# Kernel tuning notes

Hardware: AMD Instinct MI355X
Metric: run time of the kernel (lower is better)

## Reference

```python
import jax, jax.numpy as jnp
import numpy as np

N, T, D = 32, 64, 16
F = 512  # object_classes == feature dim after object_fc


def _gcn(x, adj, W, b):
    # Kipf GraphConvolution: adj @ (x @ W) + b
    return adj @ (x @ W) + b


def _norm_adj(a):
    d = jnp.sum(a, axis=1) ** -0.5
    return a * d[:, None] * d[None, :]


def _per_graph(x, gc1_W, gc1_b, gc2_W, gc2_b, gc3_W, gc3_b, gc4_W, gc4_b):
    # x: [D, F]
    # graph_generator / adj2: softmax-style similarity adjacency with D^{-1/2} norm
    s = x @ x.T                                   # [D, D]
    a = jnp.exp(s - jnp.max(s, axis=1, keepdims=True))
    adj = _norm_adj(a)
    # branch 1
    x1 = jax.nn.relu(_gcn(x, adj, gc1_W, gc1_b))
    x1 = _gcn(x1, adj, gc2_W, gc2_b)
    # branch 2 (adj_hat2 identical construction from x)
    y2 = jax.nn.relu(_gcn(x, adj, gc3_W, gc3_b))  # [D, 32]
    y22 = y2 @ y2.T
    nrm = jnp.sqrt(jnp.sum(y22 * y22, axis=1, keepdims=True))  # torch.norm(y22, 2, dim=1)
    adj3 = 1.0 + y22 / (nrm @ nrm.T)
    adj_hat3 = _norm_adj(adj3)
    y2 = _gcn(y2, adj_hat3, gc4_W, gc4_b)
    return (x1 + y2) * 0.5


def setup_inputs() -> dict:
    key = jax.random.key(0)
    ks = jax.random.split(key, 12)
    s = 0.02
    return {
        "object_raw": jax.random.normal(ks[0], (N * T * D, F), jnp.float32),
        "action_raw": jax.random.normal(ks[1], (N * T, F), jnp.float32),
        "W_obj": jax.random.normal(ks[2], (F, 512), jnp.float32) * s,
        "b_obj": jnp.zeros((512,), jnp.float32),
        "W_act": jax.random.normal(ks[3], (F, 512), jnp.float32) * s,
        "b_act": jnp.zeros((512,), jnp.float32),
        "gc1_W": jax.random.normal(ks[4], (512, 32), jnp.float32) * s,
        "gc1_b": jnp.zeros((32,), jnp.float32),
        "gc2_W": jax.random.normal(ks[5], (32, 512), jnp.float32) * s,
        "gc2_b": jnp.zeros((512,), jnp.float32),
        "gc3_W": jax.random.normal(ks[6], (512, 32), jnp.float32) * s,
        "gc3_b": jnp.zeros((32,), jnp.float32),
        "gc4_W": jax.random.normal(ks[7], (32, 512), jnp.float32) * s,
        "gc4_b": jnp.zeros((512,), jnp.float32),
        "fc1_W": jax.random.normal(ks[8], (512, 1024), jnp.float32) * s,
        "fc1_b": jnp.zeros((1024,), jnp.float32),
        "clf_W": jax.random.normal(ks[9], (1024, 500), jnp.float32) * s,
        "clf_b": jnp.zeros((500,), jnp.float32),
    }


def reference(object_raw, action_raw, W_obj, b_obj, W_act, b_act,
              gc1_W, gc1_b, gc2_W, gc2_b, gc3_W, gc3_b, gc4_W, gc4_b,
              fc1_W, fc1_b, clf_W, clf_b):
    obj = jax.nn.relu(object_raw @ W_obj + b_obj).reshape(N * T, D, 512)
    act = jax.nn.relu(action_raw @ W_act + b_act)           # [N*T, 512]
    obj = obj.at[:, D // 2].set(act)                         # overwrite middle frame
    graph = jax.vmap(lambda x: _per_graph(x, gc1_W, gc1_b, gc2_W, gc2_b,
                                          gc3_W, gc3_b, gc4_W, gc4_b))(obj)
    g = graph.reshape(N, T, D, 512).mean(axis=2)
    o = obj.reshape(N, T, D, 512).mean(axis=2)
    feat = (o + g) * 0.5                                     # graph_fusion == 'mean'
    c = jax.nn.relu(feat)                                    # dropout = identity (eval)
    c = jax.nn.relu(c @ fc1_W + fc1_b)
    out = (c @ clf_W + clf_b).mean(axis=1)                   # mean over T -> [N, 500]
    return out
```

## Files before the change

### kernel.cpp

```cpp
#include <hip/hip_runtime.h>
#include <hip/hip_bf16.h>

using ushort_t = unsigned short;
using f32x4  = __attribute__((ext_vector_type(4))) float;
using short8 = __attribute__((ext_vector_type(8))) short;

__device__ __forceinline__ float bflo(unsigned p) {
    union { unsigned u; float f; } x; x.u = p << 16; return x.f;
}
__device__ __forceinline__ float bfhi(unsigned p) {
    union { unsigned u; float f; } x; x.u = p & 0xffff0000u; return x.f;
}
__device__ __forceinline__ ushort_t f2bf(float f) {
    __hip_bfloat16 h = __float2bfloat16(f);
    return *(ushort_t*)&h;
}
__device__ __forceinline__ unsigned pk2bf(float lo, float hi) {
    __hip_bfloat162 h = __float22bfloat162_rn({lo, hi});
    return *(unsigned*)&h;
}

__device__ __forceinline__ void tr_tile(const float* __restrict__ S, ushort_t* __restrict__ D,
                                        int K, int N, int Npad, int bx, int by,
                                        int tx, int ty, float* tile )
{
    const int k0 = by * 32, n0 = bx * 32;
#pragma unroll
    for (int r = 0; r < 4; r++) {
        const int k = k0 + ty + r * 8, n = n0 + tx;
        tile[(ty + r * 8) * 33 + tx] = (k < K && n < N) ? S[(size_t)k * N + n] : 0.f;
    }
    __syncthreads();
#pragma unroll
    for (int r = 0; r < 4; r++) {
        const int n = n0 + ty + r * 8, k = k0 + tx;
        if (n < Npad && k < K) D[(size_t)n * K + k] = f2bf(tile[tx * 33 + ty + r * 8]);
    }
}

__device__ __forceinline__ void trf_tile(const float* __restrict__ S, float* __restrict__ D,
                                         int K, int N, int bx, int by,
                                         int tx, int ty, float* tile )
{
    const int k0 = by * 32, n0 = bx * 32;
#pragma unroll
    for (int r = 0; r < 4; r++) {
        const int k = k0 + ty + r * 8, n = n0 + tx;
        tile[(ty + r * 8) * 33 + tx] = (k < K && n < N) ? S[(size_t)k * N + n] : 0.f;
    }
    __syncthreads();
#pragma unroll
    for (int r = 0; r < 4; r++) {
        const int n = n0 + ty + r * 8, k = k0 + tx;
        if (n < N && k < K) D[(size_t)n * K + k] = tile[tx * 33 + ty + r * 8];
    }
}

__global__ __launch_bounds__(256)
void prep_weights(const float* __restrict__ Wobj, ushort_t* __restrict__ WobjT,
                  const float* __restrict__ Wact, ushort_t* __restrict__ WactT,
                  const float* __restrict__ fc1W, ushort_t* __restrict__ fc1T,
                  const float* __restrict__ gc1W, ushort_t* __restrict__ W1t,
                  const float* __restrict__ gc3W, ushort_t* __restrict__ W3t,
                  const float* __restrict__ gc2W, ushort_t* __restrict__ W2bf,
                  const float* __restrict__ gc4W, ushort_t* __restrict__ W4bf,
                  const float* __restrict__ clfW, float* __restrict__ WclfT)
{
    __shared__ float tile[32 * 33];
    const int b = blockIdx.x;
    const int t = threadIdx.x;
    const int tx = t & 31, ty = t >> 5;

    if (b < 1056) {
        const float* S; ushort_t* D; int K, N, Npad, nt, l;
        if      (b < 256)  { S = Wobj; D = WobjT; K = 512; N = 512;  Npad = 512;  nt = 16; l = b; }
        else if (b < 512)  { S = Wact; D = WactT; K = 512; N = 512;  Npad = 512;  nt = 16; l = b - 256; }
        else if (b < 1024) { S = fc1W; D = fc1T;  K = 512; N = 1024; Npad = 1024; nt = 32; l = b - 512; }
        else if (b < 1040) { S = gc1W; D = W1t;   K = 512; N = 32;   Npad = 32;   nt = 1;  l = b - 1024; }
        else               { S = gc3W; D = W3t;   K = 512; N = 32;   Npad = 32;   nt = 1;  l = b - 1040; }
        tr_tile(S, D, K, N, Npad, l % nt, l / nt, tx, ty, tile);
    } else if (b < 1072) {
        const float* S = (b < 1064) ? gc2W : gc4W;
        ushort_t* D    = (b < 1064) ? W2bf : W4bf;
        const int i = (b < 1064 ? b - 1056 : b - 1064) * 256 + t;
        const float4 x = ((const float4*)S)[2 * i];
        const float4 y = ((const float4*)S)[2 * i + 1];
        unsigned r[4] = { pk2bf(x.x, x.y), pk2bf(x.z, x.w), pk2bf(y.x, y.y), pk2bf(y.z, y.w) };
        ((uint4*)D)[i] = *(uint4*)r;
    } else {
        const int l = b - 1072;
        trf_tile(clfW, WclfT, 1024, 500, l & 15, l >> 4, tx, ty, tile);
    }
}

typedef __attribute__((address_space(1))) void glb_void;
typedef __attribute__((address_space(3))) void lds_void;
__device__ __forceinline__ void dma16(const void* g, void* l) {
    __builtin_amdgcn_global_load_lds((glb_void*)(unsigned long long)(uintptr_t)g,
                                     (lds_void*)(unsigned)(uintptr_t)l, 16, 0, 0);
}

template<int RELU, typename AT>
__global__ __launch_bounds__(256)
void gemm_dma(const AT* __restrict__ A, const ushort_t* __restrict__ Bt,
              const float* __restrict__ bias, ushort_t* __restrict__ C,
              int N, int K, int Nb, int row_mul, int row_add)
{
    __shared__ __align__(16) char     AsRaw[128 * 32 * sizeof(AT)];
    __shared__ __align__(16) ushort_t Bs[128 * 32];
    const int t = threadIdx.x;
    const int lane = t & 63, w = t >> 6;
    const int bm = blockIdx.y * 128, bn = blockIdx.x * 128;
    const int mb = (w & 1) * 64, nb = (w >> 1) * 64;
    const int fr = lane & 15, fq = lane >> 4;

    f32x4 acc[16];
#pragma unroll
    for (int i = 0; i < 16; i++) acc[i] = (f32x4){0.f, 0.f, 0.f, 0.f};

    const int brow = lane >> 2, bk = lane & 3;
    const int klog = bk ^ ((brow >> 1) & 3);
    const int arow = lane >> 3, ag = lane & 7;

    for (int k0 = 0; k0 < K; k0 += 32) {
        __syncthreads();
        if constexpr (sizeof(AT) == 4) {
#pragma unroll
            for (int i = 0; i < 4; i++) {
                const int grp = w * 4 + i;
                const int row = grp * 8 + arow;
                const int gl = ag ^ (row & 7);
                dma16((const float*)A + (size_t)(bm + row) * K + k0 + gl * 4,
                      AsRaw + grp * 1024);
            }
        } else {
#pragma unroll
            for (int i = 0; i < 2; i++) {
                const int grp = w * 2 + i;
                const int row = grp * 16 + brow;
                dma16((const ushort_t*)A + (size_t)(bm + row) * K + k0 + klog * 8,
                      (ushort_t*)AsRaw + grp * 512);
            }
        }
#pragma unroll
        for (int i = 0; i < 2; i++) {
            const int grp = w * 2 + i;
            const int row = grp * 16 + brow;
            dma16(Bt + (size_t)(bn + row) * K + k0 + klog * 8, Bs + grp * 512);
        }
        __syncthreads();

        short8 af[4], bf[4];
        if constexpr (sizeof(AT) == 4) {
#pragma unroll
            for (int i = 0; i < 4; i++) {
                const int row = mb + i * 16 + fr;
                const float* base = (const float*)AsRaw + row * 32;
                const f32x4 p0 = *(const f32x4*)(base + (((2 * fq)     ^ (fr & 7)) * 4));
                const f32x4 p1 = *(const f32x4*)(base + (((2 * fq + 1) ^ (fr & 7)) * 4));
                unsigned rr[4] = { pk2bf(p0.x, p0.y), pk2bf(p0.z, p0.w),
                                   pk2bf(p1.x, p1.y), pk2bf(p1.z, p1.w) };
                af[i] = *(short8*)rr;
            }
        } else {
#pragma unroll
            for (int i = 0; i < 4; i++) {
                const int row = mb + i * 16 + fr;
                af[i] = *(const short8*)((const ushort_t*)AsRaw + row * 32 + (fq ^ ((fr >> 1) & 3)) * 8);
            }
        }
#pragma unroll
        for (int j = 0; j < 4; j++) {
            const int row = nb + j * 16 + fr;
            bf[j] = *(const short8*)(Bs + row * 32 + (fq ^ ((fr >> 1) & 3)) * 8);
        }
#pragma unroll
        for (int i = 0; i < 4; i++)
#pragma unroll
            for (int j = 0; j < 4; j++)
                acc[i * 4 + j] = __builtin_amdgcn_mfma_f32_16x16x32_bf16(
                    af[i], bf[j], acc[i * 4 + j], 0, 0, 0);
    }

#pragma unroll
    for (int j = 0; j < 4; j++) {
        const int n = bn + nb + j * 16 + fr;
        const float bv = (n < Nb) ? bias[n] : 0.f;
#pragma unroll
        for (int i = 0; i < 4; i++) {
            const f32x4 a = acc[i * 4 + j];
#pragma unroll
            for (int r = 0; r < 4; r++) {
                const int m = bm + mb + i * 16 + fq * 4 + r;
                float v = a[r] + bv;
                if (RELU) v = fmaxf(v, 0.f);
                C[((size_t)m * row_mul + row_add) * (size_t)N + n] = f2bf(v);
            }
        }
    }
}

__global__ __launch_bounds__(256)
void gemm_fc1_mean(const ushort_t* __restrict__ A, const ushort_t* __restrict__ Bt,
                   const float* __restrict__ bias, float* __restrict__ cmean)
{
    __shared__ __align__(16) ushort_t AsS[128 * 32];
    __shared__ __align__(16) ushort_t Bs[128 * 32];
    const int t = threadIdx.x;
    const int lane = t & 63, w = t >> 6;
    const int bm = blockIdx.y * 128, bn = blockIdx.x * 128;
    const int mb = (w & 1) * 64, nb = (w >> 1) * 64;
    const int fr = lane & 15, fq = lane >> 4;
    const int K = 512;

    f32x4 acc[16];
#pragma unroll
    for (int i = 0; i < 16; i++) acc[i] = (f32x4){0.f, 0.f, 0.f, 0.f};

    const int brow = lane >> 2, bk = lane & 3;
    const int klog = bk ^ ((brow >> 1) & 3);

    for (int k0 = 0; k0 < K; k0 += 32) {
        __syncthreads();
#pragma unroll
        for (int i = 0; i < 2; i++) {
            const int grp = w * 2 + i;
            const int row = grp * 16 + brow;
            dma16(A + (size_t)(bm + row) * K + k0 + klog * 8, AsS + grp * 512);
        }
#pragma unroll
        for (int i = 0; i < 2; i++) {
            const int grp = w * 2 + i;
            const int row = grp * 16 + brow;
            dma16(Bt + (size_t)(bn + row) * K + k0 + klog * 8, Bs + grp * 512);
        }
        __syncthreads();

        short8 af[4], bf[4];
#pragma unroll
        for (int i = 0; i < 4; i++) {
            const int row = mb + i * 16 + fr;
            af[i] = *(const short8*)(AsS + row * 32 + (fq ^ ((fr >> 1) & 3)) * 8);
        }
#pragma unroll
        for (int j = 0; j < 4; j++) {
            const int row = nb + j * 16 + fr;
            bf[j] = *(const short8*)(Bs + row * 32 + (fq ^ ((fr >> 1) & 3)) * 8);
        }
#pragma unroll
        for (int i = 0; i < 4; i++)
#pragma unroll
            for (int j = 0; j < 4; j++)
                acc[i * 4 + j] = __builtin_amdgcn_mfma_f32_16x16x32_bf16(
                    af[i], bf[j], acc[i * 4 + j], 0, 0, 0);
    }

    const int nidx = (bm + mb) >> 6;
#pragma unroll
    for (int j = 0; j < 4; j++) {
        const int n = bn + nb + j * 16 + fr;
        const float bv = bias[n];
        float s = 0.f;
#pragma unroll
        for (int i = 0; i < 4; i++) {
            const f32x4 a = acc[i * 4 + j];
#pragma unroll
            for (int r = 0; r < 4; r++) s += fmaxf(a[r] + bv, 0.f);
        }
        s += __shfl_xor(s, 16);
        s += __shfl_xor(s, 32);
        if (fq == 0) cmean[(size_t)nidx * 1024 + n] = s * (1.0f / 64.0f);
    }
}

__global__ __launch_bounds__(512, 2)
void mega_obj_graph(const float* __restrict__ A, const ushort_t* __restrict__ Bt,
                    const float* __restrict__ bias, const ushort_t* __restrict__ act_bf,
                    const ushort_t* __restrict__ W1t, const ushort_t* __restrict__ W3t,
                    const float* __restrict__ b1, const float* __restrict__ b3,
                    const ushort_t* __restrict__ W2b, const float* __restrict__ b2,
                    const ushort_t* __restrict__ W4b, const float* __restrict__ b4,
                    ushort_t* __restrict__ cbuf)
{
    __shared__ __align__(16) ushort_t As[128 * 512];
    __shared__ __align__(16) float fsS[8][992];

    const int t = threadIdx.x;
    const int lane = t & 63, w = t >> 6;
    const int bm = blockIdx.x * 128;
    const int fr = lane & 15, fq = lane >> 4;

    const float4* A4 = (const float4*)(A + (size_t)bm * 512);
#pragma unroll
    for (int i = 0; i < 16; i++) {
        const int fl = i * 1024 + t * 2;
        const int row = fl >> 7;
        const float4 p0 = A4[fl];
        const float4 p1 = A4[fl + 1];
        unsigned rr[4] = { pk2bf(p0.x, p0.y), pk2bf(p0.z, p0.w),
                           pk2bf(p1.x, p1.y), pk2bf(p1.z, p1.w) };
        *(uint4*)&As[row * 512 + ((lane ^ (row & 7)) * 8)] = *(uint4*)rr;
    }

    const int nw = w * 64;
    const ushort_t* Bbase = Bt + (size_t)(nw + fr) * 512 + fq * 8;
    uint4 bA[4], bB[4];
#pragma unroll
    for (int j = 0; j < 4; j++) bA[j] = *(const uint4*)(Bbase + (size_t)j * 16 * 512);

    __syncthreads();

    f32x4 acc[4][8];
#pragma unroll
    for (int j = 0; j < 4; j++)
#pragma unroll
        for (int i = 0; i < 8; i++) acc[j][i] = (f32x4){0.f, 0.f, 0.f, 0.f};

    for (int kk = 0; kk < 16; kk += 2) {
        short8 af[8];
#pragma unroll
        for (int i = 0; i < 8; i++)
            af[i] = *(const short8*)&As[(i * 16 + fr) * 512 + (((kk * 4 + fq) ^ (fr & 7)) * 8)];
#pragma unroll
        for (int j = 0; j < 4; j++) {
            bB[j] = *(const uint4*)(Bbase + (size_t)j * 16 * 512 + (kk + 1) * 32);
            const short8 bf = *(const short8*)&bA[j];
#pragma unroll
            for (int i = 0; i < 8; i++)
                acc[j][i] = __builtin_amdgcn_mfma_f32_16x16x32_bf16(af[i], bf, acc[j][i], 0, 0, 0);
        }
#pragma unroll
        for (int i = 0; i < 8; i++)
            af[i] = *(const short8*)&As[(i * 16 + fr) * 512 + ((((kk + 1) * 4 + fq) ^ (fr & 7)) * 8)];
#pragma unroll
        for (int j = 0; j < 4; j++) {
            if (kk + 2 < 16)
                bA[j] = *(const uint4*)(Bbase + (size_t)j * 16 * 512 + (kk + 2) * 32);
            const short8 bf = *(const short8*)&bB[j];
#pragma unroll
            for (int i = 0; i < 8; i++)
                acc[j][i] = __builtin_amdgcn_mfma_f32_16x16x32_bf16(af[i], bf, acc[j][i], 0, 0, 0);
        }
    }

    __syncthreads();
#pragma unroll
    for (int j = 0; j < 4; j++) {
        const int col0 = j * 16 + fr;
        const float bv = bias[nw + col0];
#pragma unroll
        for (int i = 0; i < 8; i++) {
#pragma unroll
            for (int rr2 = 0; rr2 < 4; rr2++) {
                const int m = i * 16 + fq * 4 + rr2;
                const int sw = ((((col0 >> 3) ^ (m & 7)) << 3) | (col0 & 7));
                As[m * 512 + nw + sw] = f2bf(fmaxf(acc[j][i][rr2] + bv, 0.f));
            }
        }
    }
    __syncthreads();

    {
        const int ra = t >> 6, gg = t & 63;
        const uint4 v = *(const uint4*)(act_bf + (size_t)(blockIdx.x * 8 + ra) * 512 + gg * 8);
        *(uint4*)&As[(ra * 16 + 8) * 512 + gg * 8] = v;
    }
    __syncthreads();

    f32x4 e0[4], e1[4];
    float om0[8], om1[8];
    const bool isT = (w == 1) || (w == 2) || (w == 5) || (w == 6);
    const int gofs = (w >= 4) ? 4 : 0;
    const int sidx = (w == 0) ? 0 : (w == 3) ? 1 : (w == 4) ? 2 : 3;
    const int gb = sidx * 2;

    if (isT) {
        const ushort_t* Wt = ((w & 3) == 1) ? W1t : W3t;
#pragma unroll
        for (int g = 0; g < 4; g++) { e0[g] = (f32x4){0.f,0.f,0.f,0.f}; e1[g] = e0[g]; }
        for (int kk = 0; kk < 16; kk++) {
            const short8 wa = *(const short8*)(Wt + (size_t)fr * 512 + kk * 32 + fq * 8);
            const short8 wb = *(const short8*)(Wt + (size_t)(16 + fr) * 512 + kk * 32 + fq * 8);
#pragma unroll
            for (int g = 0; g < 4; g++) {
                const short8 xf = *(const short8*)&As[((gofs + g) * 16 + fr) * 512 + (((kk * 4 + fq) ^ (fr & 7)) * 8)];
                e0[g] = __builtin_amdgcn_mfma_f32_16x16x32_bf16(xf, wa, e0[g], 0, 0, 0);
                e1[g] = __builtin_amdgcn_mfma_f32_16x16x32_bf16(xf, wb, e1[g], 0, 0, 0);
            }
        }
    } else {
        e0[0] = (f32x4){0.f,0.f,0.f,0.f}; e1[0] = e0[0];
        for (int kk = 0; kk < 16; kk++) {
            const short8 xf0 = *(const short8*)&As[(gb * 16 + fr) * 512 + (((kk * 4 + fq) ^ (fr & 7)) * 8)];
            const short8 xf1 = *(const short8*)&As[((gb + 1) * 16 + fr) * 512 + (((kk * 4 + fq) ^ (fr & 7)) * 8)];
            e0[0] = __builtin_amdgcn_mfma_f32_16x16x32_bf16(xf0, xf0, e0[0], 0, 0, 0);
            e1[0] = __builtin_amdgcn_mfma_f32_16x16x32_bf16(xf1, xf1, e1[0], 0, 0, 0);
        }
#pragma unroll
        for (int c = 0; c < 8; c++) { om0[c] = 0.f; om1[c] = 0.f; }
#pragma unroll
        for (int m = 0; m < 16; m++) {
            const uint4 q0 = *(const uint4*)&As[(gb * 16 + m) * 512 + ((lane ^ (m & 7)) * 8)];
            const uint4 q1 = *(const uint4*)&As[((gb + 1) * 16 + m) * 512 + ((lane ^ (m & 7)) * 8)];
            om0[0] += bflo(q0.x); om0[1] += bfhi(q0.x);
            om0[2] += bflo(q0.y); om0[3] += bfhi(q0.y);
            om0[4] += bflo(q0.z); om0[5] += bfhi(q0.z);
            om0[6] += bflo(q0.w); om0[7] += bfhi(q0.w);
            om1[0] += bflo(q1.x); om1[1] += bfhi(q1.x);
            om1[2] += bflo(q1.y); om1[3] += bfhi(q1.y);
            om1[4] += bflo(q1.z); om1[5] += bfhi(q1.z);
            om1[6] += bflo(q1.w); om1[7] += bfhi(q1.w);
        }
    }
    __syncthreads();

    float* Hs = (float*)As;
    if (isT) {
        const int toff = ((w & 3) == 1) ? 256 : 768;
#pragma unroll
        for (int g = 0; g < 4; g++) {
            float* dst = Hs + (gofs + g) * 1792 + toff;
#pragma unroll
            for (int i = 0; i < 4; i++) {
                const int m = fq * 4 + i;
                dst[m * 32 + fr]      = e0[g][i];
                dst[m * 32 + 16 + fr] = e1[g][i];
            }
        }
    } else {
        float* d0 = Hs + gb * 1792;
        float* d1 = Hs + (gb + 1) * 1792;
#pragma unroll
        for (int i = 0; i < 4; i++) {
            const int m = fq * 4 + i;
            d0[m * 16 + fr] = e0[0][i];
            d1[m * 16 + fr] = e1[0][i];
        }
        *(float4*)(d0 + 1280 + lane * 8)     = (float4){om0[0], om0[1], om0[2], om0[3]};
        *(float4*)(d0 + 1280 + lane * 8 + 4) = (float4){om0[4], om0[5], om0[6], om0[7]};
        *(float4*)(d1 + 1280 + lane * 8)     = (float4){om1[0], om1[1], om1[2], om1[3]};
        *(float4*)(d1 + 1280 + lane * 8 + 4) = (float4){om1[4], om1[5], om1[6], om1[7]};
    }
    __syncthreads();

    {
        const int r = fr, q = fq;
        const float* Hg = Hs + w * 1792;
        float* fw   = fsS[w];
        float* adjS = fw;
        float* y2S  = fw + 272;
        float* dvS  = fw + 848;
        float* cAS  = fw + 864;
        float* nrmS = fw + 880;
        float* dv3S = fw + 896;
        float* cA3S = fw + 912;
        float* zc1S = fw + 928;
        float* zc4S = fw + 960;

        const float4 sv = *(const float4*)(Hg + r * 16 + q * 4);
        float mx = fmaxf(fmaxf(sv.x, sv.y), fmaxf(sv.z, sv.w));
        mx = fmaxf(mx, __shfl_xor(mx, 16));
        mx = fmaxf(mx, __shfl_xor(mx, 32));
        const float e0s = expf(sv.x - mx), e1s = expf(sv.y - mx);
        const float e2s = expf(sv.z - mx), e3s = expf(sv.w - mx);
        float rs = e0s + e1s + e2s + e3s;
        rs += __shfl_xor(rs, 16); rs += __shfl_xor(rs, 32);
        const float dv = rsqrtf(rs);
        if (q == 0) dvS[r] = dv;
        __syncthreads();

        float ad0, ad1, ad2, ad3;
        {
            const float4 dc = *(const float4*)&dvS[q * 4];
            ad0 = e0s * dv * dc.x; ad1 = e1s * dv * dc.y;
            ad2 = e2s * dv * dc.z; ad3 = e3s * dv * dc.w;
        }
        adjS[r * 17 + q * 4 + 0] = ad0; adjS[r * 17 + q * 4 + 1] = ad1;
        adjS[r * 17 + q * 4 + 2] = ad2; adjS[r * 17 + q * 4 + 3] = ad3;
        {
            float c0s = ad0, c1s = ad1, c2s = ad2, c3s = ad3;
#pragma unroll
            for (int m = 1; m <= 8; m <<= 1) {
                c0s += __shfl_xor(c0s, m); c1s += __shfl_xor(c1s, m);
                c2s += __shfl_xor(c2s, m); c3s += __shfl_xor(c3s, m);
            }
            if (r == 0) {
                cAS[q * 4 + 0] = c0s; cAS[q * 4 + 1] = c1s;
                cAS[q * 4 + 2] = c2s; cAS[q * 4 + 3] = c3s;
            }
        }
        __syncthreads();

        const int c0 = q * 8;
        float x1v[8], y2v[8];
        {
            const float4 b1a = *(const float4*)(b1 + c0);
            const float4 b1b = *(const float4*)(b1 + c0 + 4);
            const float4 b3a = *(const float4*)(b3 + c0);
            const float4 b3b = *(const float4*)(b3 + c0 + 4);
            x1v[0]=b1a.x; x1v[1]=b1a.y; x1v[2]=b1a.z; x1v[3]=b1a.w;
            x1v[4]=b1b.x; x1v[5]=b1b.y; x1v[6]=b1b.z; x1v[7]=b1b.w;
            y2v[0]=b3a.x; y2v[1]=b3a.y; y2v[2]=b3a.z; y2v[3]=b3a.w;
            y2v[4]=b3b.x; y2v[5]=b3b.y; y2v[6]=b3b.z; y2v[7]=b3b.w;
        }
#pragma unroll
        for (int j = 0; j < 16; j++) {
            const float a = adjS[r * 17 + j];
            const float4 t1a = *(const float4*)(Hg + 256 + j * 32 + c0);
            const float4 t1b = *(const float4*)(Hg + 256 + j * 32 + c0 + 4);
            const float4 t3a = *(const float4*)(Hg + 768 + j * 32 + c0);
            const float4 t3b = *(const float4*)(Hg + 768 + j * 32 + c0 + 4);
            x1v[0] = fmaf(a, t1a.x, x1v[0]); x1v[1] = fmaf(a, t1a.y, x1v[1]);
            x1v[2] = fmaf(a, t1a.z, x1v[2]); x1v[3] = fmaf(a, t1a.w, x1v[3]);
            x1v[4] = fmaf(a, t1b.x, x1v[4]); x1v[5] = fmaf(a, t1b.y, x1v[5]);
            x1v[6] = fmaf(a, t1b.z, x1v[6]); x1v[7] = fmaf(a, t1b.w, x1v[7]);
            y2v[0] = fmaf(a, t3a.x, y2v[0]); y2v[1] = fmaf(a, t3a.y, y2v[1]);
            y2v[2] = fmaf(a, t3a.z, y2v[2]); y2v[3] = fmaf(a, t3a.w, y2v[3]);
            y2v[4] = fmaf(a, t3b.x, y2v[4]); y2v[5] = fmaf(a, t3b.y, y2v[5]);
            y2v[6] = fmaf(a, t3b.z, y2v[6]); y2v[7] = fmaf(a, t3b.w, y2v[7]);
        }
#pragma unroll
        for (int cc = 0; cc < 8; cc++) {
            x1v[cc] = fmaxf(x1v[cc], 0.f);
            y2v[cc] = fmaxf(y2v[cc], 0.f);
            y2S[r * 36 + c0 + cc] = y2v[cc];
        }
        __syncthreads();

        float yy[4] = {0.f, 0.f, 0.f, 0.f};
#pragma unroll
        for (int k4 = 0; k4 < 8; k4++) {
            const float4 yi = *(const float4*)&y2S[r * 36 + k4 * 4];
#pragma unroll
            for (int i = 0; i < 4; i++) {
                const float4 yj = *(const float4*)&y2S[(q * 4 + i) * 36 + k4 * 4];
                yy[i] = fmaf(yi.x, yj.x, yy[i]); yy[i] = fmaf(yi.y, yj.y, yy[i]);
                yy[i] = fmaf(yi.z, yj.z, yy[i]); yy[i] = fmaf(yi.w, yj.w, yy[i]);
            }
        }
        {
            float sq = 0.f;
#pragma unroll
            for (int i = 0; i < 4; i++) sq = fmaf(yy[i], yy[i], sq);
            sq += __shfl_xor(sq, 16); sq += __shfl_xor(sq, 32);
            const float nr = sqrtf(sq);
            if (q == 0) nrmS[r] = nr;
        }
        __syncthreads();

        float a3[4];
        float dv3;
        {
            const float nr = nrmS[r];
            const float4 ncv = *(const float4*)&nrmS[q * 4];
            a3[0] = 1.0f + yy[0] / (nr * ncv.x);
            a3[1] = 1.0f + yy[1] / (nr * ncv.y);
            a3[2] = 1.0f + yy[2] / (nr * ncv.z);
            a3[3] = 1.0f + yy[3] / (nr * ncv.w);
            float d3 = a3[0] + a3[1] + a3[2] + a3[3];
            d3 += __shfl_xor(d3, 16); d3 += __shfl_xor(d3, 32);
            dv3 = rsqrtf(d3);
            if (q == 0) dv3S[r] = dv3;
        }
        {
            const float cAm = cAS[r];
            float zp[8];
#pragma unroll
            for (int cc = 0; cc < 8; cc++) zp[cc] = cAm * x1v[cc];
#pragma unroll
            for (int m = 1; m <= 8; m <<= 1)
#pragma unroll
                for (int cc = 0; cc < 8; cc++) zp[cc] += __shfl_xor(zp[cc], m);
            if (r == 0)
#pragma unroll
                for (int cc = 0; cc < 8; cc++) zc1S[c0 + cc] = zp[cc];
        }
        __syncthreads();

        {
            const float4 d3c = *(const float4*)&dv3S[q * 4];
            float p0 = a3[0] * dv3 * d3c.x, p1 = a3[1] * dv3 * d3c.y;
            float p2 = a3[2] * dv3 * d3c.z, p3 = a3[3] * dv3 * d3c.w;
#pragma unroll
            for (int m = 1; m <= 8; m <<= 1) {
                p0 += __shfl_xor(p0, m); p1 += __shfl_xor(p1, m);
                p2 += __shfl_xor(p2, m); p3 += __shfl_xor(p3, m);
            }
            if (r == 0) {
                cA3S[q * 4 + 0] = p0; cA3S[q * 4 + 1] = p1;
                cA3S[q * 4 + 2] = p2; cA3S[q * 4 + 3] = p3;
            }
        }
        __syncthreads();

        {
            const float cA3m = cA3S[r];
            float zp[8];
#pragma unroll
            for (int cc = 0; cc < 8; cc++) zp[cc] = cA3m * y2v[cc];
#pragma unroll
            for (int m = 1; m <= 8; m <<= 1)
#pragma unroll
                for (int cc = 0; cc < 8; cc++) zp[cc] += __shfl_xor(zp[cc], m);
            if (r == 0)
#pragma unroll
                for (int cc = 0; cc < 8; cc++) zc4S[c0 + cc] = zp[cc];
        }
        __syncthreads();

        {
            float gm[8] = {0,0,0,0,0,0,0,0};
            const ushort_t* w2p = W2b + lane * 8;
            const ushort_t* w4p = W4b + lane * 8;
#pragma unroll 8
            for (int k = 0; k < 32; k++) {
                const float z1 = zc1S[k], z4 = zc4S[k];
                const uint4 u2 = *(const uint4*)(w2p + (size_t)k * 512);
                const uint4 u4 = *(const uint4*)(w4p + (size_t)k * 512);
                gm[0] = fmaf(z1, bflo(u2.x), gm[0]); gm[0] = fmaf(z4, bflo(u4.x), gm[0]);
                gm[1] = fmaf(z1, bfhi(u2.x), gm[1]); gm[1] = fmaf(z4, bfhi(u4.x), gm[1]);
                gm[2] = fmaf(z1, bflo(u2.y), gm[2]); gm[2] = fmaf(z4, bflo(u4.y), gm[2]);
                gm[3] = fmaf(z1, bfhi(u2.y), gm[3]); gm[3] = fmaf(z4, bfhi(u4.y), gm[3]);
                gm[4] = fmaf(z1, bflo(u2.z), gm[4]); gm[4] = fmaf(z4, bflo(u4.z), gm[4]);
                gm[5] = fmaf(z1, bfhi(u2.z), gm[5]); gm[5] = fmaf(z4, bfhi(u4.z), gm[5]);
                gm[6] = fmaf(z1, bflo(u2.w), gm[6]); gm[6] = fmaf(z4, bflo(u4.w), gm[6]);
                gm[7] = fmaf(z1, bfhi(u2.w), gm[7]); gm[7] = fmaf(z4, bfhi(u4.w), gm[7]);
            }
            const float4 oma = *(const float4*)(Hg + 1280 + lane * 8);
            const float4 omb = *(const float4*)(Hg + 1280 + lane * 8 + 4);
            const float om[8] = {oma.x, oma.y, oma.z, oma.w, omb.x, omb.y, omb.z, omb.w};
            const float4 b2a = *(const float4*)(b2 + lane * 8);
            const float4 b2b = *(const float4*)(b2 + lane * 8 + 4);
            const float4 b4a = *(const float4*)(b4 + lane * 8);
            const float4 b4b = *(const float4*)(b4 + lane * 8 + 4);
            const float bs[8] = { b2a.x + b4a.x, b2a.y + b4a.y, b2a.z + b4a.z, b2a.w + b4a.w,
                                  b2b.x + b4b.x, b2b.y + b4b.y, b2b.z + b4b.z, b2b.w + b4b.w };
            ushort_t pk[8];
#pragma unroll
            for (int cc = 0; cc < 8; cc++) {
                const float gmean = 0.5f * bs[cc] + gm[cc] * (1.0f / 32.0f);
                const float feat  = 0.5f * (om[cc] * 0.0625f + gmean);
                pk[cc] = f2bf(fmaxf(feat, 0.f));
            }
            *(uint4*)(cbuf + (size_t)(blockIdx.x * 8 + w) * 512 + lane * 8) = *(uint4*)pk;
        }
    }
}

__global__ __launch_bounds__(256)
void clf_col(const float* __restrict__ cmean, const float* __restrict__ Wt,
             const float* __restrict__ clf_b, float* __restrict__ out)
{
    __shared__ float red[8][33];
    const int j = blockIdx.x;
    const int t = threadIdx.x;
    const int n = t & 31, kp = t >> 5;
    const float* cm = cmean + (size_t)n * 1024 + kp * 128;
    const float* wp = Wt + (size_t)j * 1024 + kp * 128;
    float acc = 0.f;
#pragma unroll
    for (int k = 0; k < 128; k += 4) {
        const float4 c = *(const float4*)(cm + k);
        const float4 wv = *(const float4*)(wp + k);
        acc = fmaf(c.x, wv.x, acc);
        acc = fmaf(c.y, wv.y, acc);
        acc = fmaf(c.z, wv.z, acc);
        acc = fmaf(c.w, wv.w, acc);
    }
    red[kp][n] = acc;
    __syncthreads();
    if (t < 32) {
        float s = red[0][t];
#pragma unroll
        for (int p = 1; p < 8; p++) s += red[p][t];
        out[(size_t)t * 500 + j] = s + clf_b[j];
    }
}

extern "C" void kernel_launch(void* const* d_in, const int* in_sizes, int n_in,
                              void* d_out, int out_size, void* d_ws, size_t ws_size,
                              hipStream_t stream)
{
    const float* object_raw = (const float*)d_in[0];
    const float* action_raw = (const float*)d_in[1];
    const float* W_obj = (const float*)d_in[2];
    const float* b_obj = (const float*)d_in[3];
    const float* W_act = (const float*)d_in[4];
    const float* b_act = (const float*)d_in[5];
    const float* gc1_W = (const float*)d_in[6];
    const float* gc1_b = (const float*)d_in[7];
    const float* gc2_W = (const float*)d_in[8];
    const float* gc2_b = (const float*)d_in[9];
    const float* gc3_W = (const float*)d_in[10];
    const float* gc3_b = (const float*)d_in[11];
    const float* gc4_W = (const float*)d_in[12];
    const float* gc4_b = (const float*)d_in[13];
    const float* fc1_W = (const float*)d_in[14];
    const float* fc1_b = (const float*)d_in[15];
    const float* clf_W = (const float*)d_in[16];
    const float* clf_b = (const float*)d_in[17];

    char* ws = (char*)d_ws;
    const size_t MB = 1024 * 1024;
    ushort_t* act_bf = (ushort_t*)(ws);
    ushort_t* cbuf   = (ushort_t*)(ws + 2 * MB);
    float*    WclfT  = (float*)   (ws + 4 * MB);
    float*    cmean  = (float*)   (ws + 6 * MB);
    ushort_t* WobjT  = (ushort_t*)(ws + 7 * MB);
    ushort_t* WactT  = (ushort_t*)(ws + 7 * MB + 512 * 1024);
    ushort_t* fc1T   = (ushort_t*)(ws + 8 * MB);
    ushort_t* W1t    = (ushort_t*)(ws + 9 * MB);
    ushort_t* W3t    = (ushort_t*)(ws + 9 * MB + 32 * 1024);
    ushort_t* W2bf   = (ushort_t*)(ws + 9 * MB + 64 * 1024);
    ushort_t* W4bf   = (ushort_t*)(ws + 9 * MB + 96 * 1024);

    prep_weights<<<dim3(1584), 256, 0, stream>>>(
        W_obj, WobjT, W_act, WactT, fc1_W, fc1T,
        gc1_W, W1t, gc3_W, W3t, gc2_W, W2bf, gc4_W, W4bf,
        clf_W, WclfT);

    gemm_dma<1, float><<<dim3(4, 16), 256, 0, stream>>>(
        action_raw, WactT, b_act, act_bf, 512, 512, 512, 1, 0);

    mega_obj_graph<<<dim3(256), 512, 0, stream>>>(
        object_raw, WobjT, b_obj, act_bf, W1t, W3t,
        gc1_b, gc3_b, W2bf, gc2_b, W4bf, gc4_b, cbuf);

    gemm_fc1_mean<<<dim3(8, 16), 256, 0, stream>>>(cbuf, fc1T, fc1_b, cmean);

    clf_col<<<dim3(500), 256, 0, stream>>>(cmean, WclfT, clf_b, (float*)d_out);
}
```

Measured before the change: 219.7 us.

## Double mega_obj_graph block to 1024 threads and rebalance per-wave work

Launches the fused object-projection/graph kernel with 16 waves per block instead of 8. In the GEMM phase each wave now owns 32 output columns instead of 64, halving its accumulator registers. In the graph phase roles are reassigned: eight waves compute the gc1/gc3 projections for one graph each, and the other eight compute the self-similarity gram and the column mean. The aim is more resident waves per CU to hide memory and MFMA latency, since LDS use allows only one block per CU. The cost is that the later per-graph phase runs on only half the waves, with extra block-wide barriers and idle waves.

```diff
diff --git a/kernel.cpp b/kernel.cpp
--- a/kernel.cpp
+++ b/kernel.cpp
@@ -273,7 +273,7 @@
     }
 }
 
-__global__ __launch_bounds__(512, 2)
+__global__ __launch_bounds__(1024, 4)
 void mega_obj_graph(const float* __restrict__ A, const ushort_t* __restrict__ Bt,
                     const float* __restrict__ bias, const ushort_t* __restrict__ act_bf,
                     const ushort_t* __restrict__ W1t, const ushort_t* __restrict__ W3t,
@@ -292,8 +292,8 @@
 
     const float4* A4 = (const float4*)(A + (size_t)bm * 512);
 #pragma unroll
-    for (int i = 0; i < 16; i++) {
-        const int fl = i * 1024 + t * 2;
+    for (int i = 0; i < 8; i++) {
+        const int fl = i * 2048 + t * 2;
         const int row = fl >> 7;
         const float4 p0 = A4[fl];
         const float4 p1 = A4[fl + 1];
@@ -302,17 +302,17 @@
         *(uint4*)&As[row * 512 + ((lane ^ (row & 7)) * 8)] = *(uint4*)rr;
     }
 
-    const int nw = w * 64;
+    const int nw = w * 32;
     const ushort_t* Bbase = Bt + (size_t)(nw + fr) * 512 + fq * 8;
-    uint4 bA[4], bB[4];
-#pragma unroll
-    for (int j = 0; j < 4; j++) bA[j] = *(const uint4*)(Bbase + (size_t)j * 16 * 512);
-
-    __syncthreads();
-
-    f32x4 acc[4][8];
-#pragma unroll
-    for (int j = 0; j < 4; j++)
+    uint4 bA[2], bB[2];
+#pragma unroll
+    for (int j = 0; j < 2; j++) bA[j] = *(const uint4*)(Bbase + (size_t)j * 16 * 512);
+
+    __syncthreads();
+
+    f32x4 acc[2][8];
+#pragma unroll
+    for (int j = 0; j < 2; j++)
 #pragma unroll
         for (int i = 0; i < 8; i++) acc[j][i] = (f32x4){0.f, 0.f, 0.f, 0.f};
 
@@ -322,7 +322,7 @@
         for (int i = 0; i < 8; i++)
             af[i] = *(const short8*)&As[(i * 16 + fr) * 512 + (((kk * 4 + fq) ^ (fr & 7)) * 8)];
 #pragma unroll
-        for (int j = 0; j < 4; j++) {
+        for (int j = 0; j < 2; j++) {
             bB[j] = *(const uint4*)(Bbase + (size_t)j * 16 * 512 + (kk + 1) * 32);
             const short8 bf = *(const short8*)&bA[j];
 #pragma unroll
@@ -333,7 +333,7 @@
         for (int i = 0; i < 8; i++)
             af[i] = *(const short8*)&As[(i * 16 + fr) * 512 + ((((kk + 1) * 4 + fq) ^ (fr & 7)) * 8)];
 #pragma unroll
-        for (int j = 0; j < 4; j++) {
+        for (int j = 0; j < 2; j++) {
             if (kk + 2 < 16)
                 bA[j] = *(const uint4*)(Bbase + (size_t)j * 16 * 512 + (kk + 2) * 32);
             const short8 bf = *(const short8*)&bB[j];
@@ -345,164 +345,141 @@
 
     __syncthreads();
 #pragma unroll
-    for (int j = 0; j < 4; j++) {
-        const int col0 = j * 16 + fr;
-        const float bv = bias[nw + col0];
+    for (int j = 0; j < 2; j++) {
+        const int col0 = nw + j * 16 + fr;
+        const float bv = bias[col0];
 #pragma unroll
         for (int i = 0; i < 8; i++) {
 #pragma unroll
             for (int rr2 = 0; rr2 < 4; rr2++) {
                 const int m = i * 16 + fq * 4 + rr2;
-                const int sw = ((((col0 >> 3) ^ (m & 7)) << 3) | (col0 & 7));
-                As[m * 512 + nw + sw] = f2bf(fmaxf(acc[j][i][rr2] + bv, 0.f));
+                As[m * 512 + ((((col0 >> 3) ^ (m & 7)) << 3) | (col0 & 7))]
+                    = f2bf(fmaxf(acc[j][i][rr2] + bv, 0.f));
             }
         }
     }
     __syncthreads();
 
-    {
+    if (t < 512) {
         const int ra = t >> 6, gg = t & 63;
         const uint4 v = *(const uint4*)(act_bf + (size_t)(blockIdx.x * 8 + ra) * 512 + gg * 8);
         *(uint4*)&As[(ra * 16 + 8) * 512 + gg * 8] = v;
     }
     __syncthreads();
 
-    f32x4 e0[4], e1[4];
-    float om0[8], om1[8];
-    const bool isT = (w == 1) || (w == 2) || (w == 5) || (w == 6);
-    const int gofs = (w >= 4) ? 4 : 0;
-    const int sidx = (w == 0) ? 0 : (w == 3) ? 1 : (w == 4) ? 2 : 3;
-    const int gb = sidx * 2;
-
-    if (isT) {
-        const ushort_t* Wt = ((w & 3) == 1) ? W1t : W3t;
-#pragma unroll
-        for (int g = 0; g < 4; g++) { e0[g] = (f32x4){0.f,0.f,0.f,0.f}; e1[g] = e0[g]; }
+    f32x4 ea = (f32x4){0.f,0.f,0.f,0.f}, eb = ea, ec = ea, ed = ea;
+    float om[8] = {0,0,0,0,0,0,0,0};
+    if (w < 8) {
         for (int kk = 0; kk < 16; kk++) {
-            const short8 wa = *(const short8*)(Wt + (size_t)fr * 512 + kk * 32 + fq * 8);
-            const short8 wb = *(const short8*)(Wt + (size_t)(16 + fr) * 512 + kk * 32 + fq * 8);
-#pragma unroll
-            for (int g = 0; g < 4; g++) {
-                const short8 xf = *(const short8*)&As[((gofs + g) * 16 + fr) * 512 + (((kk * 4 + fq) ^ (fr & 7)) * 8)];
-                e0[g] = __builtin_amdgcn_mfma_f32_16x16x32_bf16(xf, wa, e0[g], 0, 0, 0);
-                e1[g] = __builtin_amdgcn_mfma_f32_16x16x32_bf16(xf, wb, e1[g], 0, 0, 0);
-            }
+            const short8 xf = *(const short8*)&As[(w * 16 + fr) * 512 + (((kk * 4 + fq) ^ (fr & 7)) * 8)];
+            const short8 w10 = *(const short8*)(W1t + (size_t)fr * 512 + kk * 32 + fq * 8);
+            const short8 w11 = *(const short8*)(W1t + (size_t)(16 + fr) * 512 + kk * 32 + fq * 8);
+            const short8 w30 = *(const short8*)(W3t + (size_t)fr * 512 + kk * 32 + fq * 8);
+            const short8 w31 = *(const short8*)(W3t + (size_t)(16 + fr) * 512 + kk * 32 + fq * 8);
+            ea = __builtin_amdgcn_mfma_f32_16x16x32_bf16(xf, w10, ea, 0, 0, 0);
+            eb = __builtin_amdgcn_mfma_f32_16x16x32_bf16(xf, w11, eb, 0, 0, 0);
+            ec = __builtin_amdgcn_mfma_f32_16x16x32_bf16(xf, w30, ec, 0, 0, 0);
+            ed = __builtin_amdgcn_mfma_f32_16x16x32_bf16(xf, w31, ed, 0, 0, 0);
         }
     } else {
-        e0[0] = (f32x4){0.f,0.f,0.f,0.f}; e1[0] = e0[0];
+        const int g = w - 8;
         for (int kk = 0; kk < 16; kk++) {
-            const short8 xf0 = *(const short8*)&As[(gb * 16 + fr) * 512 + (((kk * 4 + fq) ^ (fr & 7)) * 8)];
-            const short8 xf1 = *(const short8*)&As[((gb + 1) * 16 + fr) * 512 + (((kk * 4 + fq) ^ (fr & 7)) * 8)];
-            e0[0] = __builtin_amdgcn_mfma_f32_16x16x32_bf16(xf0, xf0, e0[0], 0, 0, 0);
-            e1[0] = __builtin_amdgcn_mfma_f32_16x16x32_bf16(xf1, xf1, e1[0], 0, 0, 0);
-        }
-#pragma unroll
-        for (int c = 0; c < 8; c++) { om0[c] = 0.f; om1[c] = 0.f; }
+            const short8 xf = *(const short8*)&As[(g * 16 + fr) * 512 + (((kk * 4 + fq) ^ (fr & 7)) * 8)];
+            ea = __builtin_amdgcn_mfma_f32_16x16x32_bf16(xf, xf, ea, 0, 0, 0);
+        }
 #pragma unroll
         for (int m = 0; m < 16; m++) {
-            const uint4 q0 = *(const uint4*)&As[(gb * 16 + m) * 512 + ((lane ^ (m & 7)) * 8)];
-            const uint4 q1 = *(const uint4*)&As[((gb + 1) * 16 + m) * 512 + ((lane ^ (m & 7)) * 8)];
-            om0[0] += bflo(q0.x); om0[1] += bfhi(q0.x);
-            om0[2] += bflo(q0.y); om0[3] += bfhi(q0.y);
-            om0[4] += bflo(q0.z); om0[5] += bfhi(q0.z);
-            om0[6] += bflo(q0.w); om0[7] += bfhi(q0.w);
-            om1[0] += bflo(q1.x); om1[1] += bfhi(q1.x);
-            om1[2] += bflo(q1.y); om1[3] += bfhi(q1.y);
-            om1[4] += bflo(q1.z); om1[5] += bfhi(q1.z);
-            om1[6] += bflo(q1.w); om1[7] += bfhi(q1.w);
+            const uint4 q = *(const uint4*)&As[(g * 16 + m) * 512 + ((lane ^ (m & 7)) * 8)];
+            om[0] += bflo(q.x); om[1] += bfhi(q.x);
+            om[2] += bflo(q.y); om[3] += bfhi(q.y);
+            om[4] += bflo(q.z); om[5] += bfhi(q.z);
+            om[6] += bflo(q.w); om[7] += bfhi(q.w);
         }
     }
     __syncthreads();
 
     float* Hs = (float*)As;
-    if (isT) {
-        const int toff = ((w & 3) == 1) ? 256 : 768;
-#pragma unroll
-        for (int g = 0; g < 4; g++) {
-            float* dst = Hs + (gofs + g) * 1792 + toff;
-#pragma unroll
-            for (int i = 0; i < 4; i++) {
-                const int m = fq * 4 + i;
-                dst[m * 32 + fr]      = e0[g][i];
-                dst[m * 32 + 16 + fr] = e1[g][i];
-            }
-        }
-    } else {
-        float* d0 = Hs + gb * 1792;
-        float* d1 = Hs + (gb + 1) * 1792;
+    if (w < 8) {
+        float* dst = Hs + w * 1792;
 #pragma unroll
         for (int i = 0; i < 4; i++) {
             const int m = fq * 4 + i;
-            d0[m * 16 + fr] = e0[0][i];
-            d1[m * 16 + fr] = e1[0][i];
-        }
-        *(float4*)(d0 + 1280 + lane * 8)     = (float4){om0[0], om0[1], om0[2], om0[3]};
-        *(float4*)(d0 + 1280 + lane * 8 + 4) = (float4){om0[4], om0[5], om0[6], om0[7]};
-        *(float4*)(d1 + 1280 + lane * 8)     = (float4){om1[0], om1[1], om1[2], om1[3]};
-        *(float4*)(d1 + 1280 + lane * 8 + 4) = (float4){om1[4], om1[5], om1[6], om1[7]};
-    }
-    __syncthreads();
-
-    {
-        const int r = fr, q = fq;
-        const float* Hg = Hs + w * 1792;
-        float* fw   = fsS[w];
-        float* adjS = fw;
-        float* y2S  = fw + 272;
-        float* dvS  = fw + 848;
-        float* cAS  = fw + 864;
-        float* nrmS = fw + 880;
-        float* dv3S = fw + 896;
-        float* cA3S = fw + 912;
-        float* zc1S = fw + 928;
-        float* zc4S = fw + 960;
-
+            dst[256 + m * 32 + fr]      = ea[i];
+            dst[256 + m * 32 + 16 + fr] = eb[i];
+            dst[768 + m * 32 + fr]      = ec[i];
+            dst[768 + m * 32 + 16 + fr] = ed[i];
+        }
+    } else {
+        const int g = w - 8;
+        float* dst = Hs + g * 1792;
+#pragma unroll
+        for (int i = 0; i < 4; i++) {
+            const int m = fq * 4 + i;
+            dst[m * 16 + fr] = ea[i];
+        }
+        *(float4*)(dst + 1280 + lane * 8)     = (float4){om[0], om[1], om[2], om[3]};
+        *(float4*)(dst + 1280 + lane * 8 + 4) = (float4){om[4], om[5], om[6], om[7]};
+    }
+    __syncthreads();
+
+    const int r = fr, q = fq;
+    const float* Hg = Hs + (w & 7) * 1792;
+    float* fw   = fsS[w & 7];
+    float* adjS = fw;
+    float* y2S  = fw + 272;
+    float* dvS  = fw + 848;
+    float* cAS  = fw + 864;
+    float* nrmS = fw + 880;
+    float* dv3S = fw + 896;
+    float* cA3S = fw + 912;
+    float* zc1S = fw + 928;
+    float* zc4S = fw + 960;
+
+    float e0s = 0.f, e1s = 0.f, e2s = 0.f, e3s = 0.f, dv = 0.f;
+    if (w < 8) {
         const float4 sv = *(const float4*)(Hg + r * 16 + q * 4);
         float mx = fmaxf(fmaxf(sv.x, sv.y), fmaxf(sv.z, sv.w));
         mx = fmaxf(mx, __shfl_xor(mx, 16));
         mx = fmaxf(mx, __shfl_xor(mx, 32));
-        const float e0s = expf(sv.x - mx), e1s = expf(sv.y - mx);
-        const float e2s = expf(sv.z - mx), e3s = expf(sv.w - mx);
+        e0s = expf(sv.x - mx); e1s = expf(sv.y - mx);
+        e2s = expf(sv.z - mx); e3s = expf(sv.w - mx);
         float rs = e0s + e1s + e2s + e3s;
         rs += __shfl_xor(rs, 16); rs += __shfl_xor(rs, 32);
-        const float dv = rsqrtf(rs);
+        dv = rsqrtf(rs);
         if (q == 0) dvS[r] = dv;
-        __syncthreads();
-
-        float ad0, ad1, ad2, ad3;
-        {
-            const float4 dc = *(const float4*)&dvS[q * 4];
-            ad0 = e0s * dv * dc.x; ad1 = e1s * dv * dc.y;
-            ad2 = e2s * dv * dc.z; ad3 = e3s * dv * dc.w;
-        }
+    }
+    __syncthreads();
+
+    if (w < 8) {
+        const float4 dc = *(const float4*)&dvS[q * 4];
+        const float ad0 = e0s * dv * dc.x, ad1 = e1s * dv * dc.y;
+        const float ad2 = e2s * dv * dc.z, ad3 = e3s * dv * dc.w;
         adjS[r * 17 + q * 4 + 0] = ad0; adjS[r * 17 + q * 4 + 1] = ad1;
         adjS[r * 17 + q * 4 + 2] = ad2; adjS[r * 17 + q * 4 + 3] = ad3;
-        {
-            float c0s = ad0, c1s = ad1, c2s = ad2, c3s = ad3;
-#pragma unroll
-            for (int m = 1; m <= 8; m <<= 1) {
-                c0s += __shfl_xor(c0s, m); c1s += __shfl_xor(c1s, m);
-                c2s += __shfl_xor(c2s, m); c3s += __shfl_xor(c3s, m);
-            }
-            if (r == 0) {
-                cAS[q * 4 + 0] = c0s; cAS[q * 4 + 1] = c1s;
-                cAS[q * 4 + 2] = c2s; cAS[q * 4 + 3] = c3s;
-            }
-        }
-        __syncthreads();
-
-        const int c0 = q * 8;
-        float x1v[8], y2v[8];
-        {
-            const float4 b1a = *(const float4*)(b1 + c0);
-            const float4 b1b = *(const float4*)(b1 + c0 + 4);
-            const float4 b3a = *(const float4*)(b3 + c0);
-            const float4 b3b = *(const float4*)(b3 + c0 + 4);
-            x1v[0]=b1a.x; x1v[1]=b1a.y; x1v[2]=b1a.z; x1v[3]=b1a.w;
-            x1v[4]=b1b.x; x1v[5]=b1b.y; x1v[6]=b1b.z; x1v[7]=b1b.w;
-            y2v[0]=b3a.x; y2v[1]=b3a.y; y2v[2]=b3a.z; y2v[3]=b3a.w;
-            y2v[4]=b3b.x; y2v[5]=b3b.y; y2v[6]=b3b.z; y2v[7]=b3b.w;
-        }
+        float c0s = ad0, c1s = ad1, c2s = ad2, c3s = ad3;
+#pragma unroll
+        for (int m = 1; m <= 8; m <<= 1) {
+            c0s += __shfl_xor(c0s, m); c1s += __shfl_xor(c1s, m);
+            c2s += __shfl_xor(c2s, m); c3s += __shfl_xor(c3s, m);
+        }
+        if (r == 0) {
+            cAS[q * 4 + 0] = c0s; cAS[q * 4 + 1] = c1s;
+            cAS[q * 4 + 2] = c2s; cAS[q * 4 + 3] = c3s;
+        }
+    }
+    __syncthreads();
+
+    const int c0 = q * 8;
+    float x1v[8], y2v[8];
+    if (w < 8) {
+        const float4 b1a = *(const float4*)(b1 + c0);
+        const float4 b1b = *(const float4*)(b1 + c0 + 4);
+        const float4 b3a = *(const float4*)(b3 + c0);
+        const float4 b3b = *(const float4*)(b3 + c0 + 4);
+        x1v[0]=b1a.x; x1v[1]=b1a.y; x1v[2]=b1a.z; x1v[3]=b1a.w;
+        x1v[4]=b1b.x; x1v[5]=b1b.y; x1v[6]=b1b.z; x1v[7]=b1b.w;
+        y2v[0]=b3a.x; y2v[1]=b3a.y; y2v[2]=b3a.z; y2v[3]=b3a.w;
+        y2v[4]=b3b.x; y2v[5]=b3b.y; y2v[6]=b3b.z; y2v[7]=b3b.w;
 #pragma unroll
         for (int j = 0; j < 16; j++) {
             const float a = adjS[r * 17 + j];
@@ -525,9 +502,11 @@
             y2v[cc] = fmaxf(y2v[cc], 0.f);
             y2S[r * 36 + c0 + cc] = y2v[cc];
         }
-        __syncthreads();
-
-        float yy[4] = {0.f, 0.f, 0.f, 0.f};
+    }
+    __syncthreads();
+
+    float yy[4] = {0.f, 0.f, 0.f, 0.f};
+    if (w < 8) {
 #pragma unroll
         for (int k4 = 0; k4 < 8; k4++) {
             const float4 yi = *(const float4*)&y2S[r * 36 + k4 * 4];
@@ -538,112 +517,108 @@
                 yy[i] = fmaf(yi.z, yj.z, yy[i]); yy[i] = fmaf(yi.w, yj.w, yy[i]);
             }
         }
-        {
-            float sq = 0.f;
-#pragma unroll
-            for (int i = 0; i < 4; i++) sq = fmaf(yy[i], yy[i], sq);
-            sq += __shfl_xor(sq, 16); sq += __shfl_xor(sq, 32);
-            const float nr = sqrtf(sq);
-            if (q == 0) nrmS[r] = nr;
-        }
-        __syncthreads();
-
-        float a3[4];
-        float dv3;
-        {
-            const float nr = nrmS[r];
-            const float4 ncv = *(const float4*)&nrmS[q * 4];
-            a3[0] = 1.0f + yy[0] / (nr * ncv.x);
-            a3[1] = 1.0f + yy[1] / (nr * ncv.y);
-            a3[2] = 1.0f + yy[2] / (nr * ncv.z);
-            a3[3] = 1.0f + yy[3] / (nr * ncv.w);
-            float d3 = a3[0] + a3[1] + a3[2] + a3[3];
-            d3 += __shfl_xor(d3, 16); d3 += __shfl_xor(d3, 32);
-            dv3 = rsqrtf(d3);
-            if (q == 0) dv3S[r] = dv3;
-        }
-        {
-            const float cAm = cAS[r];
-            float zp[8];
-#pragma unroll
-            for (int cc = 0; cc < 8; cc++) zp[cc] = cAm * x1v[cc];
-#pragma unroll
-            for (int m = 1; m <= 8; m <<= 1)
-#pragma unroll
-                for (int cc = 0; cc < 8; cc++) zp[cc] += __shfl_xor(zp[cc], m);
-            if (r == 0)
-#pragma unroll
-                for (int cc = 0; cc < 8; cc++) zc1S[c0 + cc] = zp[cc];
-        }
-        __syncthreads();
-
-        {
-            const float4 d3c = *(const float4*)&dv3S[q * 4];
-            float p0 = a3[0] * dv3 * d3c.x, p1 = a3[1] * dv3 * d3c.y;
-            float p2 = a3[2] * dv3 * d3c.z, p3 = a3[3] * dv3 * d3c.w;
-#pragma unroll
-            for (int m = 1; m <= 8; m <<= 1) {
-                p0 += __shfl_xor(p0, m); p1 += __shfl_xor(p1, m);
-                p2 += __shfl_xor(p2, m); p3 += __shfl_xor(p3, m);
-            }
-            if (r == 0) {
-                cA3S[q * 4 + 0] = p0; cA3S[q * 4 + 1] = p1;
-                cA3S[q * 4 + 2] = p2; cA3S[q * 4 + 3] = p3;
-            }
-        }
-        __syncthreads();
-
-        {
-            const float cA3m = cA3S[r];
-            float zp[8];
-#pragma unroll
-            for (int cc = 0; cc < 8; cc++) zp[cc] = cA3m * y2v[cc];
-#pragma unroll
-            for (int m = 1; m <= 8; m <<= 1)
-#pragma unroll
-                for (int cc = 0; cc < 8; cc++) zp[cc] += __shfl_xor(zp[cc], m);
-            if (r == 0)
-#pragma unroll
-                for (int cc = 0; cc < 8; cc++) zc4S[c0 + cc] = zp[cc];
-        }
-        __syncthreads();
-
-        {
-            float gm[8] = {0,0,0,0,0,0,0,0};
-            const ushort_t* w2p = W2b + lane * 8;
-            const ushort_t* w4p = W4b + lane * 8;
+        float sq = 0.f;
+#pragma unroll
+        for (int i = 0; i < 4; i++) sq = fmaf(yy[i], yy[i], sq);
+        sq += __shfl_xor(sq, 16); sq += __shfl_xor(sq, 32);
+        const float nr = sqrtf(sq);
+        if (q == 0) nrmS[r] = nr;
+    }
+    __syncthreads();
+
+    float a3[4] = {0.f, 0.f, 0.f, 0.f};
+    float dv3 = 0.f;
+    if (w < 8) {
+        const float nr = nrmS[r];
+        const float4 ncv = *(const float4*)&nrmS[q * 4];
+        a3[0] = 1.0f + yy[0] / (nr * ncv.x);
+        a3[1] = 1.0f + yy[1] / (nr * ncv.y);
+        a3[2] = 1.0f + yy[2] / (nr * ncv.z);
+        a3[3] = 1.0f + yy[3] / (nr * ncv.w);
+        float d3 = a3[0] + a3[1] + a3[2] + a3[3];
+        d3 += __shfl_xor(d3, 16); d3 += __shfl_xor(d3, 32);
+        dv3 = rsqrtf(d3);
+        if (q == 0) dv3S[r] = dv3;
+        const float cAm = cAS[r];
+        float zp[8];
+#pragma unroll
+        for (int cc = 0; cc < 8; cc++) zp[cc] = cAm * x1v[cc];
+#pragma unroll
+        for (int m = 1; m <= 8; m <<= 1)
+#pragma unroll
+            for (int cc = 0; cc < 8; cc++) zp[cc] += __shfl_xor(zp[cc], m);
+        if (r == 0)
+#pragma unroll
+            for (int cc = 0; cc < 8; cc++) zc1S[c0 + cc] = zp[cc];
+    }
+    __syncthreads();
+
+    if (w < 8) {
+        const float4 d3c = *(const float4*)&dv3S[q * 4];
+        float p0 = a3[0] * dv3 * d3c.x, p1 = a3[1] * dv3 * d3c.y;
+        float p2 = a3[2] * dv3 * d3c.z, p3 = a3[3] * dv3 * d3c.w;
+#pragma unroll
+        for (int m = 1; m <= 8; m <<= 1) {
+            p0 += __shfl_xor(p0, m); p1 += __shfl_xor(p1, m);
+            p2 += __shfl_xor(p2, m); p3 += __shfl_xor(p3, m);
+        }
+        if (r == 0) {
+            cA3S[q * 4 + 0] = p0; cA3S[q * 4 + 1] = p1;
+            cA3S[q * 4 + 2] = p2; cA3S[q * 4 + 3] = p3;
+        }
+    }
+    __syncthreads();
+
+    if (w < 8) {
+        const float cA3m = cA3S[r];
+        float zp[8];
+#pragma unroll
+        for (int cc = 0; cc < 8; cc++) zp[cc] = cA3m * y2v[cc];
+#pragma unroll
+        for (int m = 1; m <= 8; m <<= 1)
+#pragma unroll
+            for (int cc = 0; cc < 8; cc++) zp[cc] += __shfl_xor(zp[cc], m);
+        if (r == 0)
+#pragma unroll
+            for (int cc = 0; cc < 8; cc++) zc4S[c0 + cc] = zp[cc];
+    }
+    __syncthreads();
+
+    if (w < 8) {
+        float gm[8] = {0,0,0,0,0,0,0,0};
+        const ushort_t* w2p = W2b + lane * 8;
+        const ushort_t* w4p = W4b + lane * 8;
 #pragma unroll 8
-            for (int k = 0; k < 32; k++) {
-                const float z1 = zc1S[k], z4 = zc4S[k];
-                const uint4 u2 = *(const uint4*)(w2p + (size_t)k * 512);
-                const uint4 u4 = *(const uint4*)(w4p + (size_t)k * 512);
-                gm[0] = fmaf(z1, bflo(u2.x), gm[0]); gm[0] = fmaf(z4, bflo(u4.x), gm[0]);
-                gm[1] = fmaf(z1, bfhi(u2.x), gm[1]); gm[1] = fmaf(z4, bfhi(u4.x), gm[1]);
-                gm[2] = fmaf(z1, bflo(u2.y), gm[2]); gm[2] = fmaf(z4, bflo(u4.y), gm[2]);
-                gm[3] = fmaf(z1, bfhi(u2.y), gm[3]); gm[3] = fmaf(z4, bfhi(u4.y), gm[3]);
-                gm[4] = fmaf(z1, bflo(u2.z), gm[4]); gm[4] = fmaf(z4, bflo(u4.z), gm[4]);
-                gm[5] = fmaf(z1, bfhi(u2.z), gm[5]); gm[5] = fmaf(z4, bfhi(u4.z), gm[5]);
-                gm[6] = fmaf(z1, bflo(u2.w), gm[6]); gm[6] = fmaf(z4, bflo(u4.w), gm[6]);
-                gm[7] = fmaf(z1, bfhi(u2.w), gm[7]); gm[7] = fmaf(z4, bfhi(u4.w), gm[7]);
-            }
-            const float4 oma = *(const float4*)(Hg + 1280 + lane * 8);
-            const float4 omb = *(const float4*)(Hg + 1280 + lane * 8 + 4);
-            const float om[8] = {oma.x, oma.y, oma.z, oma.w, omb.x, omb.y, omb.z, omb.w};
-            const float4 b2a = *(const float4*)(b2 + lane * 8);
-            const float4 b2b = *(const float4*)(b2 + lane * 8 + 4);
-            const float4 b4a = *(const float4*)(b4 + lane * 8);
-            const float4 b4b = *(const float4*)(b4 + lane * 8 + 4);
-            const float bs[8] = { b2a.x + b4a.x, b2a.y + b4a.y, b2a.z + b4a.z, b2a.w + b4a.w,
-                                  b2b.x + b4b.x, b2b.y + b4b.y, b2b.z + b4b.z, b2b.w + b4b.w };
-            ushort_t pk[8];
-#pragma unroll
-            for (int cc = 0; cc < 8; cc++) {
-                const float gmean = 0.5f * bs[cc] + gm[cc] * (1.0f / 32.0f);
-                const float feat  = 0.5f * (om[cc] * 0.0625f + gmean);
-                pk[cc] = f2bf(fmaxf(feat, 0.f));
-            }
-            *(uint4*)(cbuf + (size_t)(blockIdx.x * 8 + w) * 512 + lane * 8) = *(uint4*)pk;
-        }
+        for (int k = 0; k < 32; k++) {
+            const float z1 = zc1S[k], z4 = zc4S[k];
+            const uint4 u2 = *(const uint4*)(w2p + (size_t)k * 512);
+            const uint4 u4 = *(const uint4*)(w4p + (size_t)k * 512);
+            gm[0] = fmaf(z1, bflo(u2.x), gm[0]); gm[0] = fmaf(z4, bflo(u4.x), gm[0]);
+            gm[1] = fmaf(z1, bfhi(u2.x), gm[1]); gm[1] = fmaf(z4, bfhi(u4.x), gm[1]);
+            gm[2] = fmaf(z1, bflo(u2.y), gm[2]); gm[2] = fmaf(z4, bflo(u4.y), gm[2]);
+            gm[3] = fmaf(z1, bfhi(u2.y), gm[3]); gm[3] = fmaf(z4, bfhi(u4.y), gm[3]);
+            gm[4] = fmaf(z1, bflo(u2.z), gm[4]); gm[4] = fmaf(z4, bflo(u4.z), gm[4]);
+            gm[5] = fmaf(z1, bfhi(u2.z), gm[5]); gm[5] = fmaf(z4, bfhi(u4.z), gm[5]);
+            gm[6] = fmaf(z1, bflo(u2.w), gm[6]); gm[6] = fmaf(z4, bflo(u4.w), gm[6]);
+            gm[7] = fmaf(z1, bfhi(u2.w), gm[7]); gm[7] = fmaf(z4, bfhi(u4.w), gm[7]);
+        }
+        const float4 oma = *(const float4*)(Hg + 1280 + lane * 8);
+        const float4 omb = *(const float4*)(Hg + 1280 + lane * 8 + 4);
+        const float omv[8] = {oma.x, oma.y, oma.z, oma.w, omb.x, omb.y, omb.z, omb.w};
+        const float4 b2a = *(const float4*)(b2 + lane * 8);
+        const float4 b2b = *(const float4*)(b2 + lane * 8 + 4);
+        const float4 b4a = *(const float4*)(b4 + lane * 8);
+        const float4 b4b = *(const float4*)(b4 + lane * 8 + 4);
+        const float bs[8] = { b2a.x + b4a.x, b2a.y + b4a.y, b2a.z + b4a.z, b2a.w + b4a.w,
+                              b2b.x + b4b.x, b2b.y + b4b.y, b2b.z + b4b.z, b2b.w + b4b.w };
+        ushort_t pk[8];
+#pragma unroll
+        for (int cc = 0; cc < 8; cc++) {
+            const float gmean = 0.5f * bs[cc] + gm[cc] * (1.0f / 32.0f);
+            const float feat  = 0.5f * (omv[cc] * 0.0625f + gmean);
+            pk[cc] = f2bf(fmaxf(feat, 0.f));
+        }
+        *(uint4*)(cbuf + (size_t)(blockIdx.x * 8 + w) * 512 + lane * 8) = *(uint4*)pk;
     }
 }
 
@@ -722,7 +697,7 @@
     gemm_dma<1, float><<<dim3(4, 16), 256, 0, stream>>>(
         action_raw, WactT, b_act, act_bf, 512, 512, 512, 1, 0);
 
-    mega_obj_graph<<<dim3(256), 512, 0, stream>>>(
+    mega_obj_graph<<<dim3(256), 1024, 0, stream>>>(
         object_raw, WobjT, b_obj, act_bf, W1t, W3t,
         gc1_b, gc3_b, W2bf, gc2_b, W4bf, gc4_b, cbuf);
 
```

Result: no change. 222.7 us (+1.3%).
